# Optimization experiments

Hardware: AMD Instinct MI355X
Metric: run time of the kernel (lower is better)

The kernel has to match this reference:

```python
import jax, jax.numpy as jnp
import numpy as np

N_CLASSES = 64


def setup_inputs() -> dict:
    key = jax.random.key(0)
    k1, k2, k3 = jax.random.split(key, 3)
    support_embeddings = jax.random.normal(k1, (65536, 128), dtype=jnp.float32)
    support_labels = jax.random.randint(k2, (65536,), 0, N_CLASSES, dtype=jnp.int64)
    query_embeddings = jax.random.normal(k3, (262144, 128), dtype=jnp.float32)
    return {
        "support_embeddings": support_embeddings,
        "support_labels": support_labels,
        "query_embeddings": query_embeddings,
    }


def _compute_prototypes(embeddings, labels):
    # segment-mean replacing the torch per-class mask loop
    sums = jax.ops.segment_sum(embeddings, labels, num_segments=N_CLASSES)  # [C, d]
    counts = jax.ops.segment_sum(
        jnp.ones((embeddings.shape[0],), embeddings.dtype), labels, num_segments=N_CLASSES
    )  # [C]
    return sums / jnp.maximum(counts, 1.0)[:, None]


def _cdist(a, b):
    # Euclidean distance matrix [Nq, C] via ||a||^2 + ||b||^2 - 2 a.b (torch.cdist p=2)
    sq = (
        jnp.sum(a * a, axis=1, keepdims=True)
        + jnp.sum(b * b, axis=1)[None, :]
        - 2.0 * a @ b.T
    )
    return jnp.sqrt(jnp.maximum(sq, 0.0))


def reference(support_embeddings, support_labels, query_embeddings):
    prototypes = _compute_prototypes(support_embeddings, support_labels)  # [C, d]
    dists = _cdist(query_embeddings, prototypes)  # [Nq, C]
    return jax.nn.softmax(-dists, axis=1)
```

## Files before the change

### kernel.cpp

```cpp
#include <hip/hip_runtime.h>
#include <hip/hip_bf16.h>

typedef short v8s __attribute__((ext_vector_type(8)));
typedef float v4f __attribute__((ext_vector_type(4)));

#define N_SUP 65536
#define N_QRY 262144
#define DIM   128
#define NC    64

__device__ __forceinline__ unsigned short f2bf(float f) {
    union { __hip_bfloat16 h; unsigned short u; } cv;
    cv.h = __float2bfloat16(f);
    return cv.u;
}

__global__ __launch_bounds__(512)
void proto_accum(const float* __restrict__ sup, const int* __restrict__ lab,
                 float* __restrict__ part, float* __restrict__ cpart,
                 int rowsPerBlock) {
    __shared__ float cnt_s[NC];
    const int tid  = threadIdx.x;
    const int lane = tid & 63, wave = tid >> 6;
    const int l15  = lane & 15, lg = lane >> 4;

    if (tid < NC) cnt_s[tid] = 0.f;
    __syncthreads();

    const int r0blk  = blockIdx.x * rowsPerBlock;
    const int nchunk = rowsPerBlock >> 5;
    const int dt     = wave;

    v4f acc[4];
#pragma unroll
    for (int mt = 0; mt < 4; ++mt) { v4f z = {0.f, 0.f, 0.f, 0.f}; acc[mt] = z; }

    for (int ch = 0; ch < nchunk; ++ch) {
        const int r0    = r0blk + ch * 32;
        const int kbase = r0 + lg * 8;
        const int4 L0 = *(const int4*)(lab + kbase);
        const int4 L1 = *(const int4*)(lab + kbase + 4);

        if (wave == 0 && lane < 32)
            atomicAdd(&cnt_s[lab[r0 + lane]], 1.f);

        v8s A[4];
#pragma unroll
        for (int mt = 0; mt < 4; ++mt) {
            const int c = mt * 16 + l15;
            v8s a;
            a[0] = (L0.x == c) ? (short)0x3F80 : (short)0;
            a[1] = (L0.y == c) ? (short)0x3F80 : (short)0;
            a[2] = (L0.z == c) ? (short)0x3F80 : (short)0;
            a[3] = (L0.w == c) ? (short)0x3F80 : (short)0;
            a[4] = (L1.x == c) ? (short)0x3F80 : (short)0;
            a[5] = (L1.y == c) ? (short)0x3F80 : (short)0;
            a[6] = (L1.z == c) ? (short)0x3F80 : (short)0;
            a[7] = (L1.w == c) ? (short)0x3F80 : (short)0;
            A[mt] = a;
        }

        const float* ep = sup + (size_t)kbase * DIM + dt * 16 + l15;
        v8s b;
#pragma unroll
        for (int j = 0; j < 8; ++j)
            b[j] = (short)f2bf(ep[j * DIM]);

#pragma unroll
        for (int mt = 0; mt < 4; ++mt)
            acc[mt] = __builtin_amdgcn_mfma_f32_16x16x32_bf16(A[mt], b, acc[mt], 0, 0, 0);
    }

    float* pblk = part + (size_t)blockIdx.x * (NC * DIM);
#pragma unroll
    for (int mt = 0; mt < 4; ++mt)
#pragma unroll
        for (int r = 0; r < 4; ++r)
            pblk[(mt * 16 + lg * 4 + r) * DIM + dt * 16 + l15] = acc[mt][r];

    __syncthreads();
    if (tid < NC) cpart[blockIdx.x * NC + tid] = cnt_s[tid];
}

__global__ __launch_bounds__(128)
void proto_finalize(const float* __restrict__ part, const float* __restrict__ cpart,
                    unsigned short* __restrict__ pb, float* __restrict__ pp,
                    int nblk) {
    const int c = blockIdx.x, t = threadIdx.x;
    float sum = 0.f;
#pragma unroll 4
    for (int b = 0; b < nblk; ++b)
        sum += part[(size_t)b * (NC * DIM) + c * DIM + t];

    float cntf = 0.f;
#pragma unroll 4
    for (int b = 0; b < nblk; ++b)
        cntf += cpart[b * NC + c];
    const float cnt = fmaxf(cntf, 1.f);

    const float proto = sum / cnt;
    pb[c * DIM + t] = f2bf(proto);

    __shared__ float red[128];
    red[t] = proto * proto;
    __syncthreads();
    for (int s = 64; s > 0; s >>= 1) {
        if (t < s) red[t] += red[t + s];
        __syncthreads();
    }
    if (t == 0) pp[c] = red[0];
}

__global__ __launch_bounds__(256)
void fsl_main(const float* __restrict__ qry, const unsigned short* __restrict__ pb,
              const float* __restrict__ pp, float* __restrict__ out) {
    const int tid  = threadIdx.x;
    const int lane = tid & 63, wave = tid >> 6;
    const int l15  = lane & 15, lg = lane >> 4;

    v8s B[4][4];
#pragma unroll
    for (int n = 0; n < 4; ++n)
#pragma unroll
        for (int kk = 0; kk < 4; ++kk)
            B[n][kk] = *(const v8s*)(pb + (n * 16 + l15) * DIM + kk * 32 + lg * 8);

    float ppn[4];
#pragma unroll
    for (int n = 0; n < 4; ++n) ppn[n] = pp[n * 16 + l15];

    const size_t qbase = (size_t)blockIdx.x * 256 + (size_t)wave * 64;

#pragma unroll 1
    for (int m = 0; m < 4; ++m) {
        const size_t q0 = qbase + m * 16;
        const float* rowp = qry + (q0 + l15) * DIM + lg * 8;

        float qq = 0.f;
        v8s A[4];
#pragma unroll
        for (int kk = 0; kk < 4; ++kk) {
            const float4 f0 = *(const float4*)(rowp + kk * 32);
            const float4 f1 = *(const float4*)(rowp + kk * 32 + 4);
            qq = fmaf(f0.x, f0.x, qq); qq = fmaf(f0.y, f0.y, qq);
            qq = fmaf(f0.z, f0.z, qq); qq = fmaf(f0.w, f0.w, qq);
            qq = fmaf(f1.x, f1.x, qq); qq = fmaf(f1.y, f1.y, qq);
            qq = fmaf(f1.z, f1.z, qq); qq = fmaf(f1.w, f1.w, qq);
            v8s a;
            a[0] = (short)f2bf(f0.x); a[1] = (short)f2bf(f0.y);
            a[2] = (short)f2bf(f0.z); a[3] = (short)f2bf(f0.w);
            a[4] = (short)f2bf(f1.x); a[5] = (short)f2bf(f1.y);
            a[6] = (short)f2bf(f1.z); a[7] = (short)f2bf(f1.w);
            A[kk] = a;
        }
        qq += __shfl_xor(qq, 16);
        qq += __shfl_xor(qq, 32);

        v4f acc[4];
#pragma unroll
        for (int n = 0; n < 4; ++n) { v4f z = {0.f, 0.f, 0.f, 0.f}; acc[n] = z; }
#pragma unroll
        for (int kk = 0; kk < 4; ++kk)
#pragma unroll
            for (int n = 0; n < 4; ++n)
                acc[n] = __builtin_amdgcn_mfma_f32_16x16x32_bf16(A[kk], B[n][kk], acc[n], 0, 0, 0);

#pragma unroll
        for (int j = 0; j < 4; ++j) {
            const float qqj = __shfl(qq, lg * 4 + j);
            float s0 = qqj + ppn[0] - 2.f * acc[0][j];
            float s1 = qqj + ppn[1] - 2.f * acc[1][j];
            float s2 = qqj + ppn[2] - 2.f * acc[2][j];
            float s3 = qqj + ppn[3] - 2.f * acc[3][j];
            s0 = -sqrtf(fmaxf(s0, 0.f)); s1 = -sqrtf(fmaxf(s1, 0.f));
            s2 = -sqrtf(fmaxf(s2, 0.f)); s3 = -sqrtf(fmaxf(s3, 0.f));
            float mx = fmaxf(fmaxf(s0, s1), fmaxf(s2, s3));
#pragma unroll
            for (int msk = 1; msk <= 8; msk <<= 1) mx = fmaxf(mx, __shfl_xor(mx, msk));
            float e0 = __expf(s0 - mx), e1 = __expf(s1 - mx);
            float e2 = __expf(s2 - mx), e3 = __expf(s3 - mx);
            float sum = (e0 + e1) + (e2 + e3);
#pragma unroll
            for (int msk = 1; msk <= 8; msk <<= 1) sum += __shfl_xor(sum, msk);
            const float inv = __fdividef(1.f, sum);
            float* orow = out + (q0 + (size_t)lg * 4 + j) * NC;
            orow[l15]      = e0 * inv;
            orow[16 + l15] = e1 * inv;
            orow[32 + l15] = e2 * inv;
            orow[48 + l15] = e3 * inv;
        }
    }
}

extern "C" void kernel_launch(void* const* d_in, const int* in_sizes, int n_in,
                              void* d_out, int out_size, void* d_ws, size_t ws_size,
                              hipStream_t stream) {
    const float* sup = (const float*)d_in[0];
    const int*   lab = (const int*)d_in[1];
    const float* qry = (const float*)d_in[2];
    float*       out = (float*)d_out;

    auto need = [](int nb) -> size_t {
        return (size_t)nb * NC * DIM * 4 + (size_t)nb * NC * 4 + NC * DIM * 2 + NC * 4;
    };
    int nblk = 256;
    if (need(nblk) > ws_size) nblk = 128;
    if (need(nblk) > ws_size) nblk = 64;

    float*          part  = (float*)d_ws;
    float*          cpart = part + (size_t)nblk * NC * DIM;
    unsigned short* pbf   = (unsigned short*)((char*)d_ws +
                              (size_t)nblk * NC * DIM * 4 + (size_t)nblk * NC * 4);
    float*          pp    = (float*)((char*)pbf + NC * DIM * 2);

    const int rowsPerBlock = N_SUP / nblk;

    proto_accum<<<nblk, 512, 0, stream>>>(sup, lab, part, cpart, rowsPerBlock);
    proto_finalize<<<NC, 128, 0, stream>>>(part, cpart, pbf, pp, nblk);
    fsl_main<<<N_QRY / 256, 256, 0, stream>>>(qry, pbf, pp, out);
}
```

Baseline: 294.8 us.

## Transpose MFMA operands for row-contiguous softmax stores and split finalize reduction

The main kernel now computes the transposed product (prototypes as A, queries as B), so each lane holds four consecutive classes for one query row. The softmax max and sum then need only two cross-lane shuffles, and the output is written as 16-byte nontemporal vector stores instead of scalar strided stores. The main grid is changed to one 16-row tile per wave (4x more blocks, no inner m loop), which trades per-block amortisation of prototype loads for more parallelism. proto_finalize splits the partial-sum loop across 4 thread groups with a shared-memory combine to shorten the serial reduction chain.

```diff
diff --git a/kernel.cpp b/kernel.cpp
--- a/kernel.cpp
+++ b/kernel.cpp
@@ -82,30 +82,41 @@
     if (tid < NC) cpart[blockIdx.x * NC + tid] = cnt_s[tid];
 }
 
-__global__ __launch_bounds__(128)
+__global__ __launch_bounds__(512)
 void proto_finalize(const float* __restrict__ part, const float* __restrict__ cpart,
                     unsigned short* __restrict__ pb, float* __restrict__ pp,
                     int nblk) {
     const int c = blockIdx.x, t = threadIdx.x;
+    const int s = t >> 7, d = t & 127;
+    const int per = nblk >> 2;
+
     float sum = 0.f;
-#pragma unroll 4
-    for (int b = 0; b < nblk; ++b)
-        sum += part[(size_t)b * (NC * DIM) + c * DIM + t];
-
-    float cntf = 0.f;
-#pragma unroll 4
-    for (int b = 0; b < nblk; ++b)
-        cntf += cpart[b * NC + c];
-    const float cnt = fmaxf(cntf, 1.f);
-
-    const float proto = sum / cnt;
-    pb[c * DIM + t] = f2bf(proto);
-
-    __shared__ float red[128];
+    const float* pbase = part + (size_t)(s * per) * (NC * DIM) + c * DIM + d;
+#pragma unroll 8
+    for (int b = 0; b < per; ++b) sum += pbase[(size_t)b * (NC * DIM)];
+
+    float cf = 0.f;
+    const float* cbase = cpart + (size_t)(s * per) * NC + c;
+#pragma unroll 8
+    for (int b = 0; b < per; ++b) cf += cbase[(size_t)b * NC];
+
+    __shared__ float red[512];
+    __shared__ float red2[512];
+    red[t] = sum; red2[t] = cf;
+    __syncthreads();
+
+    float proto = 0.f;
+    if (t < 128) {
+        const float tot = red[t] + red[t + 128] + red[t + 256] + red[t + 384];
+        const float cnt = fmaxf(red2[t] + red2[t + 128] + red2[t + 256] + red2[t + 384], 1.f);
+        proto = tot / cnt;
+        pb[c * DIM + t] = f2bf(proto);
+    }
+    __syncthreads();
     red[t] = proto * proto;
     __syncthreads();
-    for (int s = 64; s > 0; s >>= 1) {
-        if (t < s) red[t] += red[t + s];
+    for (int st = 256; st > 0; st >>= 1) {
+        if (t < st) red[t] += red[t + st];
         __syncthreads();
     }
     if (t == 0) pp[c] = red[0];
@@ -118,77 +129,85 @@
     const int lane = tid & 63, wave = tid >> 6;
     const int l15  = lane & 15, lg = lane >> 4;
 
-    v8s B[4][4];
+    v8s PA[4][4];
 #pragma unroll
     for (int n = 0; n < 4; ++n)
 #pragma unroll
         for (int kk = 0; kk < 4; ++kk)
-            B[n][kk] = *(const v8s*)(pb + (n * 16 + l15) * DIM + kk * 32 + lg * 8);
-
-    float ppn[4];
-#pragma unroll
-    for (int n = 0; n < 4; ++n) ppn[n] = pp[n * 16 + l15];
-
-    const size_t qbase = (size_t)blockIdx.x * 256 + (size_t)wave * 64;
-
-#pragma unroll 1
-    for (int m = 0; m < 4; ++m) {
-        const size_t q0 = qbase + m * 16;
-        const float* rowp = qry + (q0 + l15) * DIM + lg * 8;
-
-        float qq = 0.f;
-        v8s A[4];
-#pragma unroll
-        for (int kk = 0; kk < 4; ++kk) {
-            const float4 f0 = *(const float4*)(rowp + kk * 32);
-            const float4 f1 = *(const float4*)(rowp + kk * 32 + 4);
-            qq = fmaf(f0.x, f0.x, qq); qq = fmaf(f0.y, f0.y, qq);
-            qq = fmaf(f0.z, f0.z, qq); qq = fmaf(f0.w, f0.w, qq);
-            qq = fmaf(f1.x, f1.x, qq); qq = fmaf(f1.y, f1.y, qq);
-            qq = fmaf(f1.z, f1.z, qq); qq = fmaf(f1.w, f1.w, qq);
-            v8s a;
-            a[0] = (short)f2bf(f0.x); a[1] = (short)f2bf(f0.y);
-            a[2] = (short)f2bf(f0.z); a[3] = (short)f2bf(f0.w);
-            a[4] = (short)f2bf(f1.x); a[5] = (short)f2bf(f1.y);
-            a[6] = (short)f2bf(f1.z); a[7] = (short)f2bf(f1.w);
-            A[kk] = a;
+            PA[n][kk] = *(const v8s*)(pb + (n * 16 + l15) * DIM + kk * 32 + lg * 8);
+
+    v4f ppv[4];
+#pragma unroll
+    for (int n = 0; n < 4; ++n)
+        ppv[n] = *(const v4f*)(pp + n * 16 + lg * 4);
+
+    const size_t q0 = (size_t)blockIdx.x * 64 + (size_t)wave * 16;
+    const float* rowp = qry + (q0 + l15) * DIM + lg * 8;
+
+    float qq = 0.f;
+    v8s QB[4];
+#pragma unroll
+    for (int kk = 0; kk < 4; ++kk) {
+        const float4 f0 = *(const float4*)(rowp + kk * 32);
+        const float4 f1 = *(const float4*)(rowp + kk * 32 + 4);
+        qq = fmaf(f0.x, f0.x, qq); qq = fmaf(f0.y, f0.y, qq);
+        qq = fmaf(f0.z, f0.z, qq); qq = fmaf(f0.w, f0.w, qq);
+        qq = fmaf(f1.x, f1.x, qq); qq = fmaf(f1.y, f1.y, qq);
+        qq = fmaf(f1.z, f1.z, qq); qq = fmaf(f1.w, f1.w, qq);
+        v8s a;
+        a[0] = (short)f2bf(f0.x); a[1] = (short)f2bf(f0.y);
+        a[2] = (short)f2bf(f0.z); a[3] = (short)f2bf(f0.w);
+        a[4] = (short)f2bf(f1.x); a[5] = (short)f2bf(f1.y);
+        a[6] = (short)f2bf(f1.z); a[7] = (short)f2bf(f1.w);
+        QB[kk] = a;
+    }
+    qq += __shfl_xor(qq, 16);
+    qq += __shfl_xor(qq, 32);
+
+    v4f acc[4];
+#pragma unroll
+    for (int n = 0; n < 4; ++n) { v4f z = {0.f, 0.f, 0.f, 0.f}; acc[n] = z; }
+#pragma unroll
+    for (int kk = 0; kk < 4; ++kk)
+#pragma unroll
+        for (int n = 0; n < 4; ++n)
+            acc[n] = __builtin_amdgcn_mfma_f32_16x16x32_bf16(PA[n][kk], QB[kk], acc[n], 0, 0, 0);
+
+    float sv[4][4];
+    float mx = -3.0e38f;
+#pragma unroll
+    for (int n = 0; n < 4; ++n)
+#pragma unroll
+        for (int r = 0; r < 4; ++r) {
+            const float d2 = qq + ppv[n][r] - 2.f * acc[n][r];
+            const float sd = -sqrtf(fmaxf(d2, 0.f));
+            sv[n][r] = sd;
+            mx = fmaxf(mx, sd);
         }
-        qq += __shfl_xor(qq, 16);
-        qq += __shfl_xor(qq, 32);
-
-        v4f acc[4];
-#pragma unroll
-        for (int n = 0; n < 4; ++n) { v4f z = {0.f, 0.f, 0.f, 0.f}; acc[n] = z; }
-#pragma unroll
-        for (int kk = 0; kk < 4; ++kk)
-#pragma unroll
-            for (int n = 0; n < 4; ++n)
-                acc[n] = __builtin_amdgcn_mfma_f32_16x16x32_bf16(A[kk], B[n][kk], acc[n], 0, 0, 0);
-
-#pragma unroll
-        for (int j = 0; j < 4; ++j) {
-            const float qqj = __shfl(qq, lg * 4 + j);
-            float s0 = qqj + ppn[0] - 2.f * acc[0][j];
-            float s1 = qqj + ppn[1] - 2.f * acc[1][j];
-            float s2 = qqj + ppn[2] - 2.f * acc[2][j];
-            float s3 = qqj + ppn[3] - 2.f * acc[3][j];
-            s0 = -sqrtf(fmaxf(s0, 0.f)); s1 = -sqrtf(fmaxf(s1, 0.f));
-            s2 = -sqrtf(fmaxf(s2, 0.f)); s3 = -sqrtf(fmaxf(s3, 0.f));
-            float mx = fmaxf(fmaxf(s0, s1), fmaxf(s2, s3));
-#pragma unroll
-            for (int msk = 1; msk <= 8; msk <<= 1) mx = fmaxf(mx, __shfl_xor(mx, msk));
-            float e0 = __expf(s0 - mx), e1 = __expf(s1 - mx);
-            float e2 = __expf(s2 - mx), e3 = __expf(s3 - mx);
-            float sum = (e0 + e1) + (e2 + e3);
-#pragma unroll
-            for (int msk = 1; msk <= 8; msk <<= 1) sum += __shfl_xor(sum, msk);
-            const float inv = __fdividef(1.f, sum);
-            float* orow = out + (q0 + (size_t)lg * 4 + j) * NC;
-            orow[l15]      = e0 * inv;
-            orow[16 + l15] = e1 * inv;
-            orow[32 + l15] = e2 * inv;
-            orow[48 + l15] = e3 * inv;
+    mx = fmaxf(mx, __shfl_xor(mx, 16));
+    mx = fmaxf(mx, __shfl_xor(mx, 32));
+
+    float sum = 0.f;
+    float ev[4][4];
+#pragma unroll
+    for (int n = 0; n < 4; ++n)
+#pragma unroll
+        for (int r = 0; r < 4; ++r) {
+            const float e = __expf(sv[n][r] - mx);
+            ev[n][r] = e;
+            sum += e;
         }
+    sum += __shfl_xor(sum, 16);
+    sum += __shfl_xor(sum, 32);
+    const float inv = __fdividef(1.f, sum);
+
+    float* orow = out + (q0 + l15) * NC;
+#pragma unroll
+    for (int n = 0; n < 4; ++n) {
+        v4f o;
+        o[0] = ev[n][0] * inv; o[1] = ev[n][1] * inv;
+        o[2] = ev[n][2] * inv; o[3] = ev[n][3] * inv;
+        __builtin_nontemporal_store(o, (v4f*)(orow + n * 16 + lg * 4));
     }
 }
 
@@ -216,6 +235,6 @@
     const int rowsPerBlock = N_SUP / nblk;
 
     proto_accum<<<nblk, 512, 0, stream>>>(sup, lab, part, cpart, rowsPerBlock);
-    proto_finalize<<<NC, 128, 0, stream>>>(part, cpart, pbf, pp, nblk);
-    fsl_main<<<N_QRY / 256, 256, 0, stream>>>(qry, pbf, pp, out);
-}
+    proto_finalize<<<NC, 512, 0, stream>>>(part, cpart, pbf, pp, nblk);
+    fsl_main<<<N_QRY / 64, 256, 0, stream>>>(qry, pbf, pp, out);
+}
```

New measurement: 264.8 us. 10.2% less time.
